# Optimization experiments

Measured on AMD Instinct MI355X. Metric: run time of the kernel, lower is better.

## Reference

```python
import jax, jax.numpy as jnp
import numpy as np

EPS = 1e-5


def conv2d(x, w, b, stride=1, pad=1):
    out = jax.lax.conv_general_dilated(
        x, w, (stride, stride), [(pad, pad), (pad, pad)],
        dimension_numbers=('NCHW', 'OIHW', 'NCHW'))
    return out + b[None, :, None, None]


def bn_inf(x, gamma, beta, mean, var):
    inv = gamma / jnp.sqrt(var + EPS)
    return x * inv[None, :, None, None] + (beta - mean * inv)[None, :, None, None]


def deform_conv(x, offset, weight, stride, pad, dil):
    # x: [B,Ci,H,W], offset: [B,2*K*K,Ho,Wo] (dy,dx interleaved per kernel pos),
    # weight: [Co,Ci,K,K]. torchvision DeformConv2d v1 semantics, no bias.
    B, Ci, H, W = x.shape
    Co, _, K, _ = weight.shape
    KK = K * K
    Ho = (H + 2 * pad - dil * (K - 1) - 1) // stride + 1
    Wo = (W + 2 * pad - dil * (K - 1) - 1) // stride + 1
    dy = offset[:, 0::2]  # [B,KK,Ho,Wo]
    dx = offset[:, 1::2]
    ky, kx = jnp.meshgrid(jnp.arange(K), jnp.arange(K), indexing='ij')
    ky = ky.reshape(KK).astype(x.dtype)
    kx = kx.reshape(KK).astype(x.dtype)
    base_y = (jnp.arange(Ho) * stride - pad).astype(x.dtype)
    base_x = (jnp.arange(Wo) * stride - pad).astype(x.dtype)
    ys = base_y[None, None, :, None] + (ky * dil)[None, :, None, None] + dy
    xs = base_x[None, None, None, :] + (kx * dil)[None, :, None, None] + dx
    y0 = jnp.floor(ys)
    x0 = jnp.floor(xs)
    fy = ys - y0
    fx = xs - x0

    def gather(img, iy, ix):
        # img: [Ci,H,W]; iy, ix: [KK,Ho,Wo] float integer-valued coords
        valid = (iy >= 0) & (iy < H) & (ix >= 0) & (ix < W)
        iyc = jnp.clip(iy, 0, H - 1).astype(jnp.int32)
        ixc = jnp.clip(ix, 0, W - 1).astype(jnp.int32)
        v = img[:, iyc, ixc]  # [Ci,KK,Ho,Wo]
        return v * valid[None].astype(img.dtype)

    def sample_one(img, y0b, x0b, fyb, fxb):
        w00 = (1 - fyb) * (1 - fxb)
        w01 = (1 - fyb) * fxb
        w10 = fyb * (1 - fxb)
        w11 = fyb * fxb
        s = (gather(img, y0b, x0b) * w00[None]
             + gather(img, y0b, x0b + 1) * w01[None]
             + gather(img, y0b + 1, x0b) * w10[None]
             + gather(img, y0b + 1, x0b + 1) * w11[None])
        return s  # [Ci,KK,Ho,Wo]

    sampled = jax.vmap(sample_one)(x, y0, x0, fy, fx)  # [B,Ci,KK,Ho,Wo]
    return jnp.einsum('oik,bikhw->bohw', weight.reshape(Co, Ci, KK), sampled)


def setup_inputs() -> dict:
    key = jax.random.key(0)
    ks = jax.random.split(key, 16)
    B, C, H, W = 8, 128, 64, 64
    d = dict(
        x=jax.random.normal(ks[0], (B, C, H, W), jnp.float32),
        w_off1=jax.random.normal(ks[1], (18, C, 3, 3), jnp.float32) * 0.01,
        b_off1=jnp.zeros((18,), jnp.float32),
        w_dc1=jax.random.normal(ks[2], (C, C, 3, 3), jnp.float32) * 0.05,
        g1=jnp.ones((C,), jnp.float32),
        beta1=jnp.zeros((C,), jnp.float32),
        m1=jax.random.normal(ks[3], (C,), jnp.float32) * 0.1,
        v1=jax.random.uniform(ks[4], (C,), jnp.float32) + 0.5,
        w_off2=jax.random.normal(ks[5], (18, C, 3, 3), jnp.float32) * 0.01,
        b_off2=jnp.zeros((18,), jnp.float32),
        w_dc2=jax.random.normal(ks[6], (C, C, 3, 3), jnp.float32) * 0.05,
        g2=jnp.ones((C,), jnp.float32),
        beta2=jnp.zeros((C,), jnp.float32),
        m2=jax.random.normal(ks[7], (C,), jnp.float32) * 0.1,
        v2=jax.random.uniform(ks[8], (C,), jnp.float32) + 0.5,
    )
    return d


def reference(x, w_off1, b_off1, w_dc1, g1, beta1, m1, v1,
              w_off2, b_off2, w_dc2, g2, beta2, m2, v2):
    # BasicBlock6 forward (stride=1, in_planes==planes => identity shortcut)
    off1 = conv2d(x, w_off1, b_off1, stride=1, pad=1)
    out = jax.nn.relu(bn_inf(deform_conv(x, off1, w_dc1, 1, 2, 2), g1, beta1, m1, v1))
    off2 = conv2d(out, w_off2, b_off2, stride=1, pad=1)
    out = bn_inf(deform_conv(out, off2, w_dc2, 1, 2, 2), g2, beta2, m2, v2)
    out = out + x  # identity shortcut
    return jax.nn.relu(out)
```

## Files before the change

kernel.cpp:

```cpp
#include <hip/hip_runtime.h>
#include <hip/hip_bf16.h>

#define CH   128
#define HH   64
#define WW   64
#define OFFC 18

typedef __attribute__((ext_vector_type(8))) short bf16x8;
typedef __attribute__((ext_vector_type(4))) short bf16x4;
typedef __attribute__((ext_vector_type(4))) float f32x4;

static __device__ __forceinline__ unsigned short f2bf(float f) {
    __hip_bfloat16 h = __float2bfloat16(f);
    return *reinterpret_cast<unsigned short*>(&h);
}
static __device__ __forceinline__ float bf2f(unsigned short u) {
    union { unsigned int i; float f; } x; x.i = ((unsigned int)u) << 16;
    return x.f;
}

__global__ __launch_bounds__(256) void prep_kernel(
    const float* __restrict__ x, unsigned short* __restrict__ xh,
    const float* __restrict__ wdc1, const float* __restrict__ wdc2,
    const float* __restrict__ wof1, const float* __restrict__ wof2,
    unsigned short* __restrict__ wpk1, unsigned short* __restrict__ wpk2,
    unsigned short* __restrict__ wpo1, unsigned short* __restrict__ wpo2)
{
    __shared__ float s[CH][WW + 1];
    int blk = blockIdx.x;
    int tid = threadIdx.x;

    if (blk < 1152) {
        const float* w = (blk < 576) ? wdc1 : wdc2;
        unsigned short* wp = (blk < 576) ? wpk1 : wpk2;
        int id = (blk % 576) * 256 + tid;
        int j    = id & 7;
        int lane = (id >> 3) & 63;
        int ot   = (id >> 9) & 7;
        int kk   = (id >> 12) & 3;
        int k    = id >> 14;
        int o = ot * 16 + (lane & 15);
        int i = kk * 32 + (lane >> 4) * 8 + j;
        wp[id] = f2bf(w[(o * CH + i) * 9 + k]);
        return;
    }
    if (blk < 1440) {
        const float* w = (blk < 1296) ? wof1 : wof2;
        unsigned short* wp = (blk < 1296) ? wpo1 : wpo2;
        int id = ((blk - 1152) % 144) * 256 + tid;
        int j    = id & 7;
        int lane = (id >> 3) & 63;
        int mt   = (id >> 9) & 1;
        int kk   = (id >> 10) & 3;
        int k    = id >> 12;
        int o = mt * 16 + (lane & 15);
        int i = kk * 32 + (lane >> 4) * 8 + j;
        wp[id] = (o < OFFC) ? f2bf(w[(o * CH + i) * 9 + k]) : (unsigned short)0;
        return;
    }

    int nb = blk - 1440;
    const float* xb = x + ((size_t)(nb >> 6) * CH * HH + (nb & 63)) * WW;

    int c_off = tid >> 4, w0 = (tid & 15) * 4;
    #pragma unroll
    for (int it = 0; it < 8; ++it) {
        int c = it * 16 + c_off;
        float4 vv = *(const float4*)&xb[(size_t)c * HH * WW + w0];
        s[c][w0] = vv.x; s[c][w0 + 1] = vv.y; s[c][w0 + 2] = vv.z; s[c][w0 + 3] = vv.w;
    }
    __syncthreads();

    int w = tid & 63, c0 = (tid >> 6) * 32;
    unsigned short* dst = xh + ((size_t)nb * WW + w) * CH + c0;
    unsigned short tmp[32];
    #pragma unroll
    for (int j = 0; j < 32; ++j) tmp[j] = f2bf(s[c0 + j][w]);
    #pragma unroll
    for (int q = 0; q < 4; ++q)
        *(bf16x8*)(dst + q * 8) = *(const bf16x8*)(tmp + q * 8);
}

__global__ __launch_bounds__(256) void off_conv_mfma_kernel(
    const unsigned short* __restrict__ xh,
    const unsigned short* __restrict__ wpo,
    const float* __restrict__ bias,
    unsigned short* __restrict__ offh)
{
    int wgid = blockIdx.x;
    int blk  = (wgid & 7) * 64 + (wgid >> 3);
    int b = blk >> 6, oh = blk & 63;
    int tid = threadIdx.x;
    int lane = tid & 63;
    int nt = tid >> 6;
    int nl = lane & 15;
    int kg = lane >> 4;

    f32x4 acc0 = {0.f, 0.f, 0.f, 0.f}, acc1 = {0.f, 0.f, 0.f, 0.f};
    const unsigned short* xb = xh + (size_t)b * HH * WW * CH;

    for (int k = 0; k < 9; ++k) {
        int ky = k / 3, kx = k - ky * 3;
        int ih = oh - 1 + ky;
        if (ih < 0 || ih >= HH) continue;
        int iw = nt * 16 + nl + kx - 1;
        bool valid = (iw >= 0) && (iw < WW);
        const unsigned short* row = xb + ((size_t)ih * WW + (valid ? iw : 0)) * CH + kg * 8;
        const unsigned short* wk = wpo + (size_t)k * 4096;
        #pragma unroll
        for (int kk = 0; kk < 4; ++kk) {
            bf16x8 bfrag = {0, 0, 0, 0, 0, 0, 0, 0};
            if (valid) bfrag = *(const bf16x8*)(row + kk * 32);
            bf16x8 a0 = *(const bf16x8*)(wk + (kk * 2 + 0) * 512 + lane * 8);
            bf16x8 a1 = *(const bf16x8*)(wk + (kk * 2 + 1) * 512 + lane * 8);
            acc0 = __builtin_amdgcn_mfma_f32_16x16x32_bf16(a0, bfrag, acc0, 0, 0, 0);
            acc1 = __builtin_amdgcn_mfma_f32_16x16x32_bf16(a1, bfrag, acc1, 0, 0, 0);
        }
    }

    int ow = nt * 16 + nl;
    #pragma unroll
    for (int r = 0; r < 4; ++r) {
        int co = kg * 4 + r;
        offh[(((size_t)b * OFFC + co) * HH + oh) * WW + ow] = f2bf(acc0[r] + bias[co]);
    }
    if (kg == 0) {
        #pragma unroll
        for (int r = 0; r < 2; ++r) {
            int co = 16 + r;
            offh[(((size_t)b * OFFC + co) * HH + oh) * WW + ow] = f2bf(acc1[r] + bias[co]);
        }
    }
}

__global__ __launch_bounds__(512, 4) void deform_pc_kernel(
    const unsigned short* __restrict__ xh,
    const unsigned short* __restrict__ offh,
    const unsigned short* __restrict__ wpk,
    const float* __restrict__ g, const float* __restrict__ beta,
    const float* __restrict__ m, const float* __restrict__ v,
    const float* __restrict__ residual,
    unsigned short* __restrict__ out_h,
    float* __restrict__ out_f)
{
    __shared__ unsigned short sB[2][64 * 128];
    __shared__ float off_s[OFFC][WW];
    __shared__ int flg[4];

    int wgid = blockIdx.x;
    int blk  = (wgid & 7) * 64 + (wgid >> 3);
    int b = blk >> 6, oh = blk & 63;
    int tid = threadIdx.x, lane = tid & 63, wv = tid >> 6;

    const unsigned short* xb = xh + (size_t)b * HH * WW * CH;

    for (int i = tid; i < OFFC * WW; i += 512) {
        int co = i >> 6, owl = i & 63;
        off_s[co][owl] =
            bf2f(offh[(((size_t)b * OFFC + co) * HH + oh) * WW + owl]);
    }
    if (tid < 4) flg[tid] = 0;
    __syncthreads();

    if (wv < 4) {
        int s_ow = tid >> 3;
        int cig  = tid & 7;

        for (int k = 0; k < 9; ++k) {
            int buf = k & 1;
            if (k >= 2) {
                int tgt = 4 * (k >> 1);
                while (__hip_atomic_load(&flg[2 + buf], __ATOMIC_ACQUIRE,
                                         __HIP_MEMORY_SCOPE_WORKGROUP) < tgt)
                    __builtin_amdgcn_s_sleep(1);
            }
            int ky = k / 3, kx = k - ky * 3;

            #pragma unroll
            for (int w2 = 0; w2 < 2; ++w2) {
                int ow = s_ow + w2 * 32;
                float dy = off_s[2 * k][ow];
                float dx = off_s[2 * k + 1][ow];
                float ys = (float)(oh - 2 + ky * 2) + dy;
                float xs = (float)(ow - 2 + kx * 2) + dx;
                float y0f = floorf(ys), x0f = floorf(xs);
                float fy = ys - y0f, fx = xs - x0f;
                int y0 = (int)y0f, x0i = (int)x0f;
                int y1 = y0 + 1, x1 = x0i + 1;
                bool vy0 = (y0 >= 0) & (y0 < HH), vy1 = (y1 >= 0) & (y1 < HH);
                bool vx0 = (x0i >= 0) & (x0i < WW), vx1 = (x1 >= 0) & (x1 < WW);
                int y0c = min(max(y0, 0), HH - 1), y1c = min(max(y1, 0), HH - 1);
                int x0c = min(max(x0i, 0), WW - 1), x1c = min(max(x1, 0), WW - 1);
                float cw0 = (1.f - fy) * (1.f - fx) * ((vy0 && vx0) ? 1.f : 0.f);
                float cw1 = (1.f - fy) * fx         * ((vy0 && vx1) ? 1.f : 0.f);
                float cw2 = fy * (1.f - fx)         * ((vy1 && vx0) ? 1.f : 0.f);
                float cw3 = fy * fx                 * ((vy1 && vx1) ? 1.f : 0.f);

                const unsigned short* p0 = xb + ((size_t)(y0c * WW + x0c)) * CH + cig * 8;
                const unsigned short* p1 = xb + ((size_t)(y0c * WW + x1c)) * CH + cig * 8;
                const unsigned short* p2 = xb + ((size_t)(y1c * WW + x0c)) * CH + cig * 8;
                const unsigned short* p3 = xb + ((size_t)(y1c * WW + x1c)) * CH + cig * 8;

                int swz = (ow & 7) << 4;
                #pragma unroll
                for (int q = 0; q < 2; ++q) {
                    int cie = q * 64 + cig * 8;
                    bf16x8 g0 = *(const bf16x8*)(p0 + q * 64);
                    bf16x8 g1 = *(const bf16x8*)(p1 + q * 64);
                    bf16x8 g2 = *(const bf16x8*)(p2 + q * 64);
                    bf16x8 g3 = *(const bf16x8*)(p3 + q * 64);
                    union { bf16x8 v8; unsigned short u[8]; } wu;
                    #pragma unroll
                    for (int j = 0; j < 8; ++j) {
                        float val = cw0 * bf2f((unsigned short)g0[j])
                                  + cw1 * bf2f((unsigned short)g1[j])
                                  + cw2 * bf2f((unsigned short)g2[j])
                                  + cw3 * bf2f((unsigned short)g3[j]);
                        wu.u[j] = f2bf(val);
                    }
                    int byte = (ow * 256 + cie * 2) ^ swz;
                    *(bf16x8*)((char*)sB[buf] + byte) = wu.v8;
                }
            }
            asm volatile("s_waitcnt lgkmcnt(0)" ::: "memory");
            if (lane == 0)
                __hip_atomic_fetch_add(&flg[buf], 1, __ATOMIC_RELEASE,
                                       __HIP_MEMORY_SCOPE_WORKGROUP);
        }
    } else {
        int cw = wv - 4;
        f32x4 acc[2][4];
        #pragma unroll
        for (int a = 0; a < 2; ++a)
            #pragma unroll
            for (int q = 0; q < 4; ++q) acc[a][q] = (f32x4){0.f, 0.f, 0.f, 0.f};

        for (int k = 0; k < 9; ++k) {
            int buf = k & 1;
            int tgt = 4 * ((k >> 1) + 1);
            while (__hip_atomic_load(&flg[buf], __ATOMIC_ACQUIRE,
                                     __HIP_MEMORY_SCOPE_WORKGROUP) < tgt)
                __builtin_amdgcn_s_sleep(1);

            const unsigned short* wk = wpk + (size_t)k * 16384;
            __builtin_amdgcn_s_setprio(1);
            #pragma unroll
            for (int kk = 0; kk < 4; ++kk) {
                bf16x8 a0 = *(const bf16x8*)(wk + (size_t)(kk * 8 + 2 * cw)     * 512 + lane * 8);
                bf16x8 a1 = *(const bf16x8*)(wk + (size_t)(kk * 8 + 2 * cw + 1) * 512 + lane * 8);
                #pragma unroll
                for (int owt = 0; owt < 4; ++owt) {
                    int owl = owt * 16 + (lane & 15);
                    int rbyte = (owl * 256 + (kk * 32 + (lane >> 4) * 8) * 2)
                                ^ ((owl & 7) << 4);
                    bf16x8 bfv = *(const bf16x8*)((const char*)sB[buf] + rbyte);
                    acc[0][owt] = __builtin_amdgcn_mfma_f32_16x16x32_bf16(
                                      a0, bfv, acc[0][owt], 0, 0, 0);
                    acc[1][owt] = __builtin_amdgcn_mfma_f32_16x16x32_bf16(
                                      a1, bfv, acc[1][owt], 0, 0, 0);
                }
            }
            __builtin_amdgcn_s_setprio(0);
            asm volatile("s_waitcnt lgkmcnt(0)" ::: "memory");
            if (lane == 0)
                __hip_atomic_fetch_add(&flg[2 + buf], 1, __ATOMIC_RELEASE,
                                       __HIP_MEMORY_SCOPE_WORKGROUP);
        }

        #pragma unroll
        for (int otl = 0; otl < 2; ++otl) {
            int ob = (2 * cw + otl) * 16 + (lane >> 4) * 4;
            float inv[4], sh[4];
            #pragma unroll
            for (int r = 0; r < 4; ++r) {
                int o = ob + r;
                float iv = g[o] / sqrtf(v[o] + 1e-5f);
                inv[r] = iv; sh[r] = beta[o] - m[o] * iv;
            }
            if (out_h != nullptr) {
                #pragma unroll
                for (int owt = 0; owt < 4; ++owt) {
                    int ow = owt * 16 + (lane & 15);
                    union { bf16x4 v4; unsigned short u[4]; } pk;
                    #pragma unroll
                    for (int r = 0; r < 4; ++r) {
                        float val = acc[otl][owt][r] * inv[r] + sh[r];
                        pk.u[r] = f2bf(fmaxf(val, 0.f));
                    }
                    *(bf16x4*)(out_h + ((size_t)(b * HH + oh) * WW + ow) * CH + ob) = pk.v4;
                }
            } else {
                #pragma unroll
                for (int r = 0; r < 4; ++r) {
                    int o = ob + r;
                    #pragma unroll
                    for (int owt = 0; owt < 4; ++owt) {
                        int ow = owt * 16 + (lane & 15);
                        size_t idx = (((size_t)b * CH + o) * HH + oh) * WW + ow;
                        float val = acc[otl][owt][r] * inv[r] + sh[r] + residual[idx];
                        out_f[idx] = fmaxf(val, 0.f);
                    }
                }
            }
        }
    }
}

extern "C" void kernel_launch(void* const* d_in, const int* in_sizes, int n_in,
                              void* d_out, int out_size, void* d_ws, size_t ws_size,
                              hipStream_t stream)
{
    const float* x      = (const float*)d_in[0];
    const float* w_off1 = (const float*)d_in[1];
    const float* b_off1 = (const float*)d_in[2];
    const float* w_dc1  = (const float*)d_in[3];
    const float* g1     = (const float*)d_in[4];
    const float* beta1  = (const float*)d_in[5];
    const float* m1     = (const float*)d_in[6];
    const float* v1     = (const float*)d_in[7];
    const float* w_off2 = (const float*)d_in[8];
    const float* b_off2 = (const float*)d_in[9];
    const float* w_dc2  = (const float*)d_in[10];
    const float* g2     = (const float*)d_in[11];
    const float* beta2  = (const float*)d_in[12];
    const float* m2     = (const float*)d_in[13];
    const float* v2     = (const float*)d_in[14];
    float* out = (float*)d_out;

    char* ws = (char*)d_ws;
    unsigned short* xh    = (unsigned short*)ws;
    unsigned short* out1h = (unsigned short*)(ws + 8388608);
    unsigned short* offh  = (unsigned short*)(ws + 16777216);
    unsigned short* wpk1  = (unsigned short*)(ws + 17956864);
    unsigned short* wpk2  = (unsigned short*)(ws + 18251776);
    unsigned short* wpo1  = (unsigned short*)(ws + 18546688);
    unsigned short* wpo2  = (unsigned short*)(ws + 18620416);

    prep_kernel<<<1952, 256, 0, stream>>>(x, xh, w_dc1, w_dc2, w_off1, w_off2,
                                          wpk1, wpk2, wpo1, wpo2);

    off_conv_mfma_kernel<<<512, 256, 0, stream>>>(xh, wpo1, b_off1, offh);
    deform_pc_kernel<<<512, 512, 0, stream>>>(xh, offh, wpk1,
                                              g1, beta1, m1, v1,
                                              nullptr, out1h, nullptr);
    off_conv_mfma_kernel<<<512, 256, 0, stream>>>(out1h, wpo2, b_off2, offh);
    deform_pc_kernel<<<512, 512, 0, stream>>>(out1h, offh, wpk2,
                                              g2, beta2, m2, v2,
                                              x, nullptr, out);
}
```

Measured before the change: 91.56 us.

## Software-pipeline gather loads and weight fragment loads one tap ahead

The producer waves now compute coordinates for the next kernel tap and issue its eight global gather loads before waiting on the buffer flag, then blend the prefetched data. The consumer waves likewise prefetch the next tap's weight fragments into registers after the MFMA loop. The aim is to hide global load latency behind the spin-wait and compute, at the cost of more live registers, which under launch_bounds(512,4) could cause spills.

```diff
diff --git a/kernel.cpp b/kernel.cpp
--- a/kernel.cpp
+++ b/kernel.cpp
@@ -133,6 +133,65 @@
     }
 }
 
+#define P_COORD(K, OW, CW, PTR) do {                                          \
+    int ky_ = (K) / 3, kx_ = (K) - ky_ * 3;                                   \
+    float dy_ = off_s[2 * (K)][OW];                                           \
+    float dx_ = off_s[2 * (K) + 1][OW];                                       \
+    float ys_ = (float)(oh - 2 + ky_ * 2) + dy_;                              \
+    float xs_ = (float)((OW) - 2 + kx_ * 2) + dx_;                            \
+    float y0f_ = floorf(ys_), x0f_ = floorf(xs_);                             \
+    float fy_ = ys_ - y0f_, fx_ = xs_ - x0f_;                                 \
+    int y0_ = (int)y0f_, x0_ = (int)x0f_;                                     \
+    int y1_ = y0_ + 1, x1_ = x0_ + 1;                                         \
+    bool vy0_ = (y0_ >= 0) & (y0_ < HH), vy1_ = (y1_ >= 0) & (y1_ < HH);      \
+    bool vx0_ = (x0_ >= 0) & (x0_ < WW), vx1_ = (x1_ >= 0) & (x1_ < WW);      \
+    int y0c_ = min(max(y0_, 0), HH - 1), y1c_ = min(max(y1_, 0), HH - 1);     \
+    int x0c_ = min(max(x0_, 0), WW - 1), x1c_ = min(max(x1_, 0), WW - 1);     \
+    CW[0] = (1.f - fy_) * (1.f - fx_) * ((vy0_ && vx0_) ? 1.f : 0.f);         \
+    CW[1] = (1.f - fy_) * fx_         * ((vy0_ && vx1_) ? 1.f : 0.f);         \
+    CW[2] = fy_ * (1.f - fx_)         * ((vy1_ && vx0_) ? 1.f : 0.f);         \
+    CW[3] = fy_ * fx_                 * ((vy1_ && vx1_) ? 1.f : 0.f);         \
+    PTR[0] = xb + ((size_t)(y0c_ * WW + x0c_)) * CH + cig * 8;                \
+    PTR[1] = xb + ((size_t)(y0c_ * WW + x1c_)) * CH + cig * 8;                \
+    PTR[2] = xb + ((size_t)(y1c_ * WW + x0c_)) * CH + cig * 8;                \
+    PTR[3] = xb + ((size_t)(y1c_ * WW + x1c_)) * CH + cig * 8;                \
+} while (0)
+
+#define P_ISSUE(PTR, LD) do {                                                 \
+    _Pragma("unroll")                                                         \
+    for (int c_ = 0; c_ < 4; ++c_) {                                          \
+        LD[0][c_] = *(const bf16x8*)(PTR[c_]);                                \
+        LD[1][c_] = *(const bf16x8*)(PTR[c_] + 64);                           \
+    }                                                                         \
+} while (0)
+
+#define P_BLEND(OW, CW, LD, BUF) do {                                         \
+    int swz_ = ((OW) & 7) << 4;                                               \
+    _Pragma("unroll")                                                         \
+    for (int q_ = 0; q_ < 2; ++q_) {                                          \
+        union { bf16x8 v8; unsigned short u[8]; } wu_;                        \
+        _Pragma("unroll")                                                     \
+        for (int j_ = 0; j_ < 8; ++j_) {                                      \
+            float val_ = CW[0] * bf2f((unsigned short)LD[q_][0][j_])          \
+                       + CW[1] * bf2f((unsigned short)LD[q_][1][j_])          \
+                       + CW[2] * bf2f((unsigned short)LD[q_][2][j_])          \
+                       + CW[3] * bf2f((unsigned short)LD[q_][3][j_]);         \
+            wu_.u[j_] = f2bf(val_);                                           \
+        }                                                                     \
+        int byte_ = ((OW) * 256 + (q_ * 64 + cig * 8) * 2) ^ swz_;            \
+        *(bf16x8*)((char*)sB[BUF] + byte_) = wu_.v8;                          \
+    }                                                                         \
+} while (0)
+
+#define C_PREF(K, AP) do {                                                    \
+    const unsigned short* wk_ = wpk + (size_t)(K) * 16384;                    \
+    _Pragma("unroll")                                                         \
+    for (int kk_ = 0; kk_ < 4; ++kk_) {                                       \
+        AP[kk_ * 2 + 0] = *(const bf16x8*)(wk_ + (size_t)(kk_ * 8 + 2 * cwi)     * 512 + lane * 8); \
+        AP[kk_ * 2 + 1] = *(const bf16x8*)(wk_ + (size_t)(kk_ * 8 + 2 * cwi + 1) * 512 + lane * 8); \
+    }                                                                         \
+} while (0)
+
 __global__ __launch_bounds__(512, 4) void deform_pc_kernel(
     const unsigned short* __restrict__ xh,
     const unsigned short* __restrict__ offh,
@@ -166,6 +225,15 @@
         int s_ow = tid >> 3;
         int cig  = tid & 7;
 
+        float cwA[4], cwB[4];
+        const unsigned short *ptA[4], *ptB[4];
+        bf16x8 ldA[2][4], ldB[2][4];
+
+        P_COORD(0, s_ow, cwA, ptA);
+        P_COORD(0, s_ow + 32, cwB, ptB);
+        P_ISSUE(ptA, ldA);
+        P_ISSUE(ptB, ldB);
+
         for (int k = 0; k < 9; ++k) {
             int buf = k & 1;
             if (k >= 2) {
@@ -174,66 +242,29 @@
                                          __HIP_MEMORY_SCOPE_WORKGROUP) < tgt)
                     __builtin_amdgcn_s_sleep(1);
             }
-            int ky = k / 3, kx = k - ky * 3;
-
-            #pragma unroll
-            for (int w2 = 0; w2 < 2; ++w2) {
-                int ow = s_ow + w2 * 32;
-                float dy = off_s[2 * k][ow];
-                float dx = off_s[2 * k + 1][ow];
-                float ys = (float)(oh - 2 + ky * 2) + dy;
-                float xs = (float)(ow - 2 + kx * 2) + dx;
-                float y0f = floorf(ys), x0f = floorf(xs);
-                float fy = ys - y0f, fx = xs - x0f;
-                int y0 = (int)y0f, x0i = (int)x0f;
-                int y1 = y0 + 1, x1 = x0i + 1;
-                bool vy0 = (y0 >= 0) & (y0 < HH), vy1 = (y1 >= 0) & (y1 < HH);
-                bool vx0 = (x0i >= 0) & (x0i < WW), vx1 = (x1 >= 0) & (x1 < WW);
-                int y0c = min(max(y0, 0), HH - 1), y1c = min(max(y1, 0), HH - 1);
-                int x0c = min(max(x0i, 0), WW - 1), x1c = min(max(x1, 0), WW - 1);
-                float cw0 = (1.f - fy) * (1.f - fx) * ((vy0 && vx0) ? 1.f : 0.f);
-                float cw1 = (1.f - fy) * fx         * ((vy0 && vx1) ? 1.f : 0.f);
-                float cw2 = fy * (1.f - fx)         * ((vy1 && vx0) ? 1.f : 0.f);
-                float cw3 = fy * fx                 * ((vy1 && vx1) ? 1.f : 0.f);
-
-                const unsigned short* p0 = xb + ((size_t)(y0c * WW + x0c)) * CH + cig * 8;
-                const unsigned short* p1 = xb + ((size_t)(y0c * WW + x1c)) * CH + cig * 8;
-                const unsigned short* p2 = xb + ((size_t)(y1c * WW + x0c)) * CH + cig * 8;
-                const unsigned short* p3 = xb + ((size_t)(y1c * WW + x1c)) * CH + cig * 8;
-
-                int swz = (ow & 7) << 4;
-                #pragma unroll
-                for (int q = 0; q < 2; ++q) {
-                    int cie = q * 64 + cig * 8;
-                    bf16x8 g0 = *(const bf16x8*)(p0 + q * 64);
-                    bf16x8 g1 = *(const bf16x8*)(p1 + q * 64);
-                    bf16x8 g2 = *(const bf16x8*)(p2 + q * 64);
-                    bf16x8 g3 = *(const bf16x8*)(p3 + q * 64);
-                    union { bf16x8 v8; unsigned short u[8]; } wu;
-                    #pragma unroll
-                    for (int j = 0; j < 8; ++j) {
-                        float val = cw0 * bf2f((unsigned short)g0[j])
-                                  + cw1 * bf2f((unsigned short)g1[j])
-                                  + cw2 * bf2f((unsigned short)g2[j])
-                                  + cw3 * bf2f((unsigned short)g3[j]);
-                        wu.u[j] = f2bf(val);
-                    }
-                    int byte = (ow * 256 + cie * 2) ^ swz;
-                    *(bf16x8*)((char*)sB[buf] + byte) = wu.v8;
-                }
-            }
+            P_BLEND(s_ow,      cwA, ldA, buf);
+            P_BLEND(s_ow + 32, cwB, ldB, buf);
             asm volatile("s_waitcnt lgkmcnt(0)" ::: "memory");
             if (lane == 0)
                 __hip_atomic_fetch_add(&flg[buf], 1, __ATOMIC_RELEASE,
                                        __HIP_MEMORY_SCOPE_WORKGROUP);
+            if (k < 8) {
+                P_COORD(k + 1, s_ow, cwA, ptA);
+                P_COORD(k + 1, s_ow + 32, cwB, ptB);
+                P_ISSUE(ptA, ldA);
+                P_ISSUE(ptB, ldB);
+            }
         }
     } else {
-        int cw = wv - 4;
+        int cwi = wv - 4;
         f32x4 acc[2][4];
         #pragma unroll
         for (int a = 0; a < 2; ++a)
             #pragma unroll
             for (int q = 0; q < 4; ++q) acc[a][q] = (f32x4){0.f, 0.f, 0.f, 0.f};
+
+        bf16x8 aP[8];
+        C_PREF(0, aP);
 
         for (int k = 0; k < 9; ++k) {
             int buf = k & 1;
@@ -242,12 +273,9 @@
                                      __HIP_MEMORY_SCOPE_WORKGROUP) < tgt)
                 __builtin_amdgcn_s_sleep(1);
 
-            const unsigned short* wk = wpk + (size_t)k * 16384;
             __builtin_amdgcn_s_setprio(1);
             #pragma unroll
             for (int kk = 0; kk < 4; ++kk) {
-                bf16x8 a0 = *(const bf16x8*)(wk + (size_t)(kk * 8 + 2 * cw)     * 512 + lane * 8);
-                bf16x8 a1 = *(const bf16x8*)(wk + (size_t)(kk * 8 + 2 * cw + 1) * 512 + lane * 8);
                 #pragma unroll
                 for (int owt = 0; owt < 4; ++owt) {
                     int owl = owt * 16 + (lane & 15);
@@ -255,9 +283,9 @@
                                 ^ ((owl & 7) << 4);
                     bf16x8 bfv = *(const bf16x8*)((const char*)sB[buf] + rbyte);
                     acc[0][owt] = __builtin_amdgcn_mfma_f32_16x16x32_bf16(
-                                      a0, bfv, acc[0][owt], 0, 0, 0);
+                                      aP[kk * 2 + 0], bfv, acc[0][owt], 0, 0, 0);
                     acc[1][owt] = __builtin_amdgcn_mfma_f32_16x16x32_bf16(
-                                      a1, bfv, acc[1][owt], 0, 0, 0);
+                                      aP[kk * 2 + 1], bfv, acc[1][owt], 0, 0, 0);
                 }
             }
             __builtin_amdgcn_s_setprio(0);
@@ -265,11 +293,12 @@
             if (lane == 0)
                 __hip_atomic_fetch_add(&flg[2 + buf], 1, __ATOMIC_RELEASE,
                                        __HIP_MEMORY_SCOPE_WORKGROUP);
+            if (k < 8) C_PREF(k + 1, aP);
         }
 
         #pragma unroll
         for (int otl = 0; otl < 2; ++otl) {
-            int ob = (2 * cw + otl) * 16 + (lane >> 4) * 4;
+            int ob = (2 * cwi + otl) * 16 + (lane >> 4) * 4;
             float inv[4], sh[4];
             #pragma unroll
             for (int r = 0; r < 4; ++r) {
```

Result: no change. 90.65 us (-1.0%).
